# Performance work log

Measured on AMD Instinct MI355X. Metric: run time of the kernel, lower is better.

Reference implementation:

```python
import jax, jax.numpy as jnp
import numpy as np

B, N, M = 4, 2048, 2048
QUERY_DIM = 512
CONTEXT_DIM = 512
HEADS = 8
DIM_HEAD = 64
INNER = HEADS * DIM_HEAD  # 512
SCALE = DIM_HEAD ** -0.5


def setup_inputs() -> dict:
    key = jax.random.key(0)
    ks = jax.random.split(key, 7)
    x = jax.random.normal(ks[0], (B, N, QUERY_DIM), dtype=jnp.float32)
    context = jax.random.normal(ks[1], (B, M, CONTEXT_DIM), dtype=jnp.float32)
    mask = jax.random.randint(ks[2], (B, M), 0, 2) > 0  # bool key mask
    # Kaiming-uniform-ish init scale, like nn.Linear defaults
    Wq = jax.random.uniform(ks[3], (QUERY_DIM, INNER), dtype=jnp.float32,
                            minval=-1, maxval=1) * (QUERY_DIM ** -0.5)
    Wkv = jax.random.uniform(ks[4], (CONTEXT_DIM, 2 * INNER), dtype=jnp.float32,
                             minval=-1, maxval=1) * (CONTEXT_DIM ** -0.5)
    Wo = jax.random.uniform(ks[5], (INNER, QUERY_DIM), dtype=jnp.float32,
                            minval=-1, maxval=1) * (INNER ** -0.5)
    bo = jax.random.uniform(ks[6], (QUERY_DIM,), dtype=jnp.float32,
                            minval=-1, maxval=1) * (INNER ** -0.5)
    return {"x": x, "context": context, "mask": mask,
            "Wq": Wq, "Wkv": Wkv, "Wo": Wo, "bo": bo}


def reference(x, context, mask, Wq, Wkv, Wo, bo):
    # projections (no bias for q/kv, bias for out — as in the torch module)
    q = x @ Wq                       # [b, n, inner]
    kv = context @ Wkv               # [b, m, 2*inner]
    k, v = jnp.split(kv, 2, axis=-1)
    # split heads: b n (h d) -> b h n d
    def split_heads(t):
        b, n, _ = t.shape
        return t.reshape(b, n, HEADS, DIM_HEAD).transpose(0, 2, 1, 3)
    q, k, v = split_heads(q), split_heads(k), split_heads(v)
    sim = jnp.einsum('bhid,bhjd->bhij', q, k) * SCALE  # [b, h, n, m]
    max_neg = -jnp.finfo(sim.dtype).max
    sim = jnp.where(mask[:, None, None, :], sim, max_neg)
    attn = jax.nn.softmax(sim, axis=-1)
    out = jnp.einsum('bhij,bhjd->bhid', attn, v)       # [b, h, n, d]
    out = out.transpose(0, 2, 1, 3).reshape(x.shape[0], x.shape[1], INNER)
    return out @ Wo + bo
```

## Files before the change

### kernel.cpp

```cpp
#include <hip/hip_runtime.h>
#include <hip/hip_bf16.h>
#include <cstddef>

typedef __attribute__((ext_vector_type(8))) short short8;
typedef __attribute__((ext_vector_type(4))) float f32x4;

__device__ inline unsigned short f2bf(float f) {
  unsigned int u = __float_as_uint(f);
  u += 0x7fffu + ((u >> 16) & 1u);
  return (unsigned short)(u >> 16);
}
__device__ inline unsigned int pkbf(float a, float b) {
  __hip_bfloat162 h = __float22bfloat162_rn(make_float2(a, b));
  union { __hip_bfloat162 h2; unsigned int u; } cv;
  cv.h2 = h;
  return cv.u;
}

__global__ __launch_bounds__(256) void prep_kernel(
    const float* __restrict__ Wq, const float* __restrict__ Wkv,
    const float* __restrict__ Wo, const int* __restrict__ mask,
    unsigned short* __restrict__ Wq_t, unsigned short* __restrict__ Wkv_t,
    unsigned short* __restrict__ Wo_t, unsigned int* __restrict__ pmask) {
  const int z = blockIdx.z;
  if (z == 3) {
    if (blockIdx.y != 0) return;
    int idx = blockIdx.x * 256 + threadIdx.x;
    int bb = idx >> 10, rem = idx & 1023;
    int g = rem >> 5, rem2 = rem & 31;
    int lqv = rem2 >> 3, e = rem2 & 7;
    int ct = e >> 1, half = e & 1;
    int key0 = g * 64 + half * 32 + lqv * 8 + 2 * ct;
    const int* mb = mask + bb * 2048;
    pmask[idx] = (mb[key0] ? 0xFFFFu : 0u) | (mb[key0 + 1] ? 0xFFFF0000u : 0u);
    return;
  }
  const float* src = (z == 0) ? Wq : (z == 1) ? Wkv : Wo;
  unsigned short* dst = (z == 0) ? Wq_t : (z == 1) ? Wkv_t : Wo_t;
  const int R = 512, C = (z == 1) ? 1024 : 512;
  if (blockIdx.x * 64 >= C) return;
  __shared__ float tile[64][65];
  int c0 = blockIdx.x * 64, r0 = blockIdx.y * 64;
  int tx = threadIdx.x & 63, ty = threadIdx.x >> 6;
  for (int i = ty; i < 64; i += 4)
    tile[i][tx] = src[(size_t)(r0 + i) * C + c0 + tx];
  __syncthreads();
  for (int i = ty; i < 64; i += 4)
    dst[(size_t)(c0 + i) * R + r0 + tx] = f2bf(tile[tx][i]);
}

__global__ __launch_bounds__(256) void proj_kernel(
    const float* __restrict__ x, const float* __restrict__ context,
    const unsigned short* __restrict__ Wq_t, const unsigned short* __restrict__ Wkv_t,
    unsigned short* __restrict__ qb, unsigned short* __restrict__ kb,
    unsigned short* __restrict__ vtb, float qscale) {
  __shared__ unsigned short As[128][72];
  __shared__ unsigned short Bs[128][72];
  const int bid = blockIdx.x;
  const bool isq = bid < 256;
  const int lid = isq ? bid : bid - 256;
  const float* Af = isq ? x : context;
  const unsigned short* Bt = isq ? Wq_t : Wkv_t;
  const int bn = (isq ? (lid & 3) : (lid & 7)) * 128;
  const int bm = (isq ? (lid >> 2) : (lid >> 3)) * 128;
  const int K = 512;
  const int tid = threadIdx.x;
  const int wave = tid >> 6, lane = tid & 63;
  const int wr = (wave >> 1) * 64, wc = (wave & 1) * 64;
  const int l15 = lane & 15, lq = lane >> 4;
  const int sr = tid >> 3, sc = (tid & 7) * 8;
  f32x4 acc[4][4] = {};

  for (int k0 = 0; k0 < K; k0 += 64) {
    __syncthreads();
#pragma unroll
    for (int p = 0; p < 4; ++p) {
      int r = sr + p * 32;
      const float4 f0 = *(const float4*)(Af + (size_t)(bm + r) * K + k0 + sc);
      const float4 f1 = *(const float4*)(Af + (size_t)(bm + r) * K + k0 + sc + 4);
      uint4 u;
      u.x = pkbf(f0.x, f0.y);
      u.y = pkbf(f0.z, f0.w);
      u.z = pkbf(f1.x, f1.y);
      u.w = pkbf(f1.z, f1.w);
      *(uint4*)(&As[r][sc]) = u;
      *(uint4*)(&Bs[r][sc]) = *(const uint4*)(Bt + (size_t)(bn + r) * K + k0 + sc);
    }
    __syncthreads();
#pragma unroll
    for (int kk = 0; kk < 2; ++kk) {
      short8 af[4], bfr[4];
#pragma unroll
      for (int mt = 0; mt < 4; ++mt)
        af[mt] = *(const short8*)(&As[wr + mt * 16 + l15][kk * 32 + lq * 8]);
#pragma unroll
      for (int nt = 0; nt < 4; ++nt)
        bfr[nt] = *(const short8*)(&Bs[wc + nt * 16 + l15][kk * 32 + lq * 8]);
#pragma unroll
      for (int mt = 0; mt < 4; ++mt)
#pragma unroll
        for (int nt = 0; nt < 4; ++nt)
          acc[mt][nt] = __builtin_amdgcn_mfma_f32_16x16x32_bf16(af[mt], bfr[nt], acc[mt][nt], 0, 0, 0);
    }
  }

#pragma unroll
  for (int mt = 0; mt < 4; ++mt)
#pragma unroll
    for (int nt = 0; nt < 4; ++nt) {
      int row0 = bm + wr + mt * 16 + lq * 4;
      int col = bn + wc + nt * 16 + l15;
      if (isq) {
#pragma unroll
        for (int j = 0; j < 4; ++j)
          qb[(size_t)(row0 + j) * 512 + col] = f2bf(acc[mt][nt][j] * qscale);
      } else if (col < 512) {
#pragma unroll
        for (int j = 0; j < 4; ++j)
          kb[(size_t)(row0 + j) * 512 + col] = f2bf(acc[mt][nt][j]);
      } else {
        int bb = row0 >> 11, m = row0 & 2047;
        int hd = col - 512;
        uint2 w;
        w.x = pkbf(acc[mt][nt][0], acc[mt][nt][1]);
        w.y = pkbf(acc[mt][nt][2], acc[mt][nt][3]);
        *(uint2*)(vtb + ((size_t)bb * 512 + hd) * 2048 + m) = w;
      }
    }
}

__global__ __launch_bounds__(256) void outproj_kernel(
    const unsigned short* __restrict__ Ab, const unsigned short* __restrict__ Bt,
    float* __restrict__ C0, const float* __restrict__ bias) {
  __shared__ unsigned short As[64][72];
  __shared__ unsigned short Bs[128][72];
  const int bm = blockIdx.y * 64, bn = blockIdx.x * 128;
  const int K = 512, N = 512;
  const int tid = threadIdx.x;
  const int wave = tid >> 6, lane = tid & 63;
  const int wr = (wave >> 1) * 32, wc = (wave & 1) * 64;
  const int l15 = lane & 15, lq = lane >> 4;
  const int sr = tid >> 3, sc = (tid & 7) * 8;
  f32x4 acc[2][4] = {};

  for (int k0 = 0; k0 < K; k0 += 64) {
    __syncthreads();
#pragma unroll
    for (int p = 0; p < 2; ++p)
      *(uint4*)(&As[sr + p * 32][sc]) = *(const uint4*)(Ab + (size_t)(bm + sr + p * 32) * K + k0 + sc);
#pragma unroll
    for (int p = 0; p < 4; ++p)
      *(uint4*)(&Bs[sr + p * 32][sc]) = *(const uint4*)(Bt + (size_t)(bn + sr + p * 32) * K + k0 + sc);
    __syncthreads();
#pragma unroll
    for (int kk = 0; kk < 2; ++kk) {
      short8 af[2], bfr[4];
#pragma unroll
      for (int mt = 0; mt < 2; ++mt)
        af[mt] = *(const short8*)(&As[wr + mt * 16 + l15][kk * 32 + lq * 8]);
#pragma unroll
      for (int nt = 0; nt < 4; ++nt)
        bfr[nt] = *(const short8*)(&Bs[wc + nt * 16 + l15][kk * 32 + lq * 8]);
#pragma unroll
      for (int mt = 0; mt < 2; ++mt)
#pragma unroll
        for (int nt = 0; nt < 4; ++nt)
          acc[mt][nt] = __builtin_amdgcn_mfma_f32_16x16x32_bf16(af[mt], bfr[nt], acc[mt][nt], 0, 0, 0);
    }
  }

#pragma unroll
  for (int mt = 0; mt < 2; ++mt)
#pragma unroll
    for (int nt = 0; nt < 4; ++nt) {
      int row0 = bm + wr + mt * 16 + lq * 4;
      int col = bn + wc + nt * 16 + l15;
#pragma unroll
      for (int j = 0; j < 4; ++j)
        C0[(size_t)(row0 + j) * N + col] = acc[mt][nt][j] + bias[col];
    }
}

__global__ __launch_bounds__(256, 3) void attn_kernel(
    const unsigned short* __restrict__ Q, const unsigned short* __restrict__ Kb,
    const unsigned short* __restrict__ Vt, const unsigned int* __restrict__ pmask,
    unsigned short* __restrict__ O) {
  __shared__ unsigned short Ks[2][64][72];
  __shared__ unsigned short Vs[2][64][72];
  const int b = blockIdx.x >> 3, h = blockIdx.x & 7;
  const int tid = threadIdx.x, lane = tid & 63;
  const int wave = tid >> 6;
  const int l15 = lane & 15, lq = lane >> 4;
  const int wrow = blockIdx.y * 128 + wave * 32;

  const unsigned short* Qr0 = Q + (size_t)(b * 2048 + wrow + l15) * 512 + h * 64;
  const unsigned short* Qr1 = Q + (size_t)(b * 2048 + wrow + 16 + l15) * 512 + h * 64;
  short8 q00 = *(const short8*)(Qr0 + lq * 8);
  short8 q01 = *(const short8*)(Qr0 + 32 + lq * 8);
  short8 q10 = *(const short8*)(Qr1 + lq * 8);
  short8 q11 = *(const short8*)(Qr1 + 32 + lq * 8);

  const short8 vones = {0x3F80, 0x3F80, 0x3F80, 0x3F80,
                        0x3F80, 0x3F80, 0x3F80, 0x3F80};

  f32x4 o0[4] = {}, o1[4] = {};
  f32x4 ol0 = {}, ol1 = {};

  const unsigned short* Kg = Kb + (size_t)b * 2048 * 512 + h * 64;
  const unsigned short* Vg = Vt + (size_t)(b * 8 + h) * 64 * 2048;
  const unsigned int* Pm = pmask + b * 1024;

  const int str = tid >> 3;
  const int stc = (tid & 7) * 8;
  const int kprow = ((str & 7) >> 1) * 16 + ((str >> 3) & 3) * 4 + (str & 1);

  uint4 krA0 = *(const uint4*)(Kg + (size_t)str * 512 + stc);
  uint4 krA1 = *(const uint4*)(Kg + (size_t)(str + 32) * 512 + stc);
  uint4 krB0 = *(const uint4*)(Kg + (size_t)(64 + str) * 512 + stc);
  uint4 krB1 = *(const uint4*)(Kg + (size_t)(64 + str + 32) * 512 + stc);
  uint4 vrA0 = *(const uint4*)(Vg + (size_t)str * 2048 + stc);
  uint4 vrA1 = *(const uint4*)(Vg + (size_t)(str + 32) * 2048 + stc);
  uint4 vrB0 = *(const uint4*)(Vg + (size_t)str * 2048 + 64 + stc);
  uint4 vrB1 = *(const uint4*)(Vg + (size_t)(str + 32) * 2048 + 64 + stc);

  for (int mb = 0; mb < 2048; mb += 128) {
    __syncthreads();
    *(uint4*)(&Ks[0][kprow][stc])     = krA0;
    *(uint4*)(&Ks[0][kprow + 2][stc]) = krA1;
    *(uint4*)(&Ks[1][kprow][stc])     = krB0;
    *(uint4*)(&Ks[1][kprow + 2][stc]) = krB1;
    *(uint4*)(&Vs[0][str][stc])       = vrA0;
    *(uint4*)(&Vs[0][str + 32][stc])  = vrA1;
    *(uint4*)(&Vs[1][str][stc])       = vrB0;
    *(uint4*)(&Vs[1][str + 32][stc])  = vrB1;
    __syncthreads();
    if (mb + 128 < 2048) {
      const int nx = mb + 128;
      krA0 = *(const uint4*)(Kg + (size_t)(nx + str) * 512 + stc);
      krA1 = *(const uint4*)(Kg + (size_t)(nx + str + 32) * 512 + stc);
      krB0 = *(const uint4*)(Kg + (size_t)(nx + 64 + str) * 512 + stc);
      krB1 = *(const uint4*)(Kg + (size_t)(nx + 64 + str + 32) * 512 + stc);
      vrA0 = *(const uint4*)(Vg + (size_t)str * 2048 + nx + stc);
      vrA1 = *(const uint4*)(Vg + (size_t)(str + 32) * 2048 + nx + stc);
      vrB0 = *(const uint4*)(Vg + (size_t)str * 2048 + nx + 64 + stc);
      vrB1 = *(const uint4*)(Vg + (size_t)(str + 32) * 2048 + nx + 64 + stc);
    }

#pragma unroll
    for (int g = 0; g < 2; ++g) {
      const uint4 m0 = *(const uint4*)(Pm + ((mb >> 6) + g) * 32 + lq * 8);
      const uint4 m1 = *(const uint4*)(Pm + ((mb >> 6) + g) * 32 + lq * 8 + 4);

      f32x4 s0[4] = {}, s1[4] = {};
      __builtin_amdgcn_s_setprio(1);
#pragma unroll
      for (int ct = 0; ct < 4; ++ct) {
        short8 kf = *(const short8*)(&Ks[g][ct * 16 + l15][lq * 8]);
        s0[ct] = __builtin_amdgcn_mfma_f32_16x16x32_bf16(kf, q00, s0[ct], 0, 0, 0);
        s1[ct] = __builtin_amdgcn_mfma_f32_16x16x32_bf16(kf, q10, s1[ct], 0, 0, 0);
      }
#pragma unroll
      for (int ct = 0; ct < 4; ++ct) {
        short8 kf = *(const short8*)(&Ks[g][ct * 16 + l15][32 + lq * 8]);
        s0[ct] = __builtin_amdgcn_mfma_f32_16x16x32_bf16(kf, q01, s0[ct], 0, 0, 0);
        s1[ct] = __builtin_amdgcn_mfma_f32_16x16x32_bf16(kf, q11, s1[ct], 0, 0, 0);
      }
      __builtin_amdgcn_s_setprio(0);

      unsigned int xp0[4][2], xp1[4][2];
#pragma unroll
      for (int ct = 0; ct < 4; ++ct) {
        float a0 = __builtin_amdgcn_exp2f(s0[ct][0]);
        float a1 = __builtin_amdgcn_exp2f(s0[ct][1]);
        float a2 = __builtin_amdgcn_exp2f(s0[ct][2]);
        float a3 = __builtin_amdgcn_exp2f(s0[ct][3]);
        xp0[ct][0] = pkbf(a0, a1);
        xp0[ct][1] = pkbf(a2, a3);
        float c0 = __builtin_amdgcn_exp2f(s1[ct][0]);
        float c1 = __builtin_amdgcn_exp2f(s1[ct][1]);
        float c2 = __builtin_amdgcn_exp2f(s1[ct][2]);
        float c3 = __builtin_amdgcn_exp2f(s1[ct][3]);
        xp1[ct][0] = pkbf(c0, c1);
        xp1[ct][1] = pkbf(c2, c3);
      }

      xp0[0][0] &= m0.x; xp0[0][1] &= m0.y; xp0[1][0] &= m0.z; xp0[1][1] &= m0.w;
      xp0[2][0] &= m1.x; xp0[2][1] &= m1.y; xp0[3][0] &= m1.z; xp0[3][1] &= m1.w;
      xp1[0][0] &= m0.x; xp1[0][1] &= m0.y; xp1[1][0] &= m0.z; xp1[1][1] &= m0.w;
      xp1[2][0] &= m1.x; xp1[2][1] &= m1.y; xp1[3][0] &= m1.z; xp1[3][1] &= m1.w;

      __builtin_amdgcn_s_setprio(1);
#pragma unroll
      for (int kk = 0; kk < 2; ++kk) {
        union { unsigned int u[4]; short8 s8; } pc0, pc1;
        pc0.u[0] = xp0[0][kk]; pc0.u[1] = xp0[1][kk];
        pc0.u[2] = xp0[2][kk]; pc0.u[3] = xp0[3][kk];
        pc1.u[0] = xp1[0][kk]; pc1.u[1] = xp1[1][kk];
        pc1.u[2] = xp1[2][kk]; pc1.u[3] = xp1[3][kk];
#pragma unroll
        for (int dt = 0; dt < 4; ++dt) {
          short8 vf = *(const short8*)(&Vs[g][dt * 16 + l15][kk * 32 + lq * 8]);
          o0[dt] = __builtin_amdgcn_mfma_f32_16x16x32_bf16(vf, pc0.s8, o0[dt], 0, 0, 0);
          o1[dt] = __builtin_amdgcn_mfma_f32_16x16x32_bf16(vf, pc1.s8, o1[dt], 0, 0, 0);
        }
        ol0 = __builtin_amdgcn_mfma_f32_16x16x32_bf16(vones, pc0.s8, ol0, 0, 0, 0);
        ol1 = __builtin_amdgcn_mfma_f32_16x16x32_bf16(vones, pc1.s8, ol1, 0, 0, 0);
      }
      __builtin_amdgcn_s_setprio(0);
    }
  }

  float rl0 = 1.0f / ol0[0], rl1 = 1.0f / ol1[0];
  unsigned short* Or0 = O + (size_t)(b * 2048 + wrow + l15) * 512 + h * 64;
  unsigned short* Or1 = O + (size_t)(b * 2048 + wrow + 16 + l15) * 512 + h * 64;
#pragma unroll
  for (int dt = 0; dt < 4; ++dt) {
    *(unsigned int*)(Or0 + dt * 16 + lq * 4)     = pkbf(o0[dt][0] * rl0, o0[dt][1] * rl0);
    *(unsigned int*)(Or0 + dt * 16 + lq * 4 + 2) = pkbf(o0[dt][2] * rl0, o0[dt][3] * rl0);
    *(unsigned int*)(Or1 + dt * 16 + lq * 4)     = pkbf(o1[dt][0] * rl1, o1[dt][1] * rl1);
    *(unsigned int*)(Or1 + dt * 16 + lq * 4 + 2) = pkbf(o1[dt][2] * rl1, o1[dt][3] * rl1);
  }
}

extern "C" void kernel_launch(void* const* d_in, const int* in_sizes, int n_in,
                              void* d_out, int out_size, void* d_ws, size_t ws_size,
                              hipStream_t stream) {
  const float* x       = (const float*)d_in[0];
  const float* context = (const float*)d_in[1];
  const int*   mask    = (const int*)d_in[2];
  const float* Wq      = (const float*)d_in[3];
  const float* Wkv     = (const float*)d_in[4];
  const float* Wo      = (const float*)d_in[5];
  const float* bo      = (const float*)d_in[6];
  float* out = (float*)d_out;

  char* ws = (char*)d_ws;
  unsigned short* Wq_t  = (unsigned short*)(ws + 0);
  unsigned short* Wkv_t = (unsigned short*)(ws + 524288);
  unsigned short* Wo_t  = (unsigned short*)(ws + 1572864);
  unsigned short* qb    = (unsigned short*)(ws + 2097152);
  unsigned short* kb    = (unsigned short*)(ws + 10485760);
  unsigned short* vtb   = (unsigned short*)(ws + 18874368);
  unsigned short* ab    = (unsigned short*)(ws + 27262976);
  unsigned int* pmask   = (unsigned int*)(ws + 35651584);

  const float QSCALE = 0.125f * 1.44269504088896f;

  prep_kernel<<<dim3(16, 8, 4), 256, 0, stream>>>(Wq, Wkv, Wo, mask,
                                                  Wq_t, Wkv_t, Wo_t, pmask);
  proj_kernel<<<dim3(768), 256, 0, stream>>>(x, context, Wq_t, Wkv_t,
                                             qb, kb, vtb, QSCALE);
  attn_kernel<<<dim3(32, 16), 256, 0, stream>>>(qb, kb, vtb, pmask, ab);
  outproj_kernel<<<dim3(4, 128), 256, 0, stream>>>(ab, Wo_t, out, bo);
}
```

Before: 106.5 us.

## Split attention over key halves and merge partials in output projection

The attention kernel is split along the key dimension into two halves (grid z=2), each writing unnormalized bf16 partial outputs and row sums. The output projection then merges the two partials and normalizes while loading its A tile. Launch bounds rise to 4 blocks per CU and the setprio hints are removed. This doubles the number of attention blocks to fill more CUs, at the cost of extra partial-output traffic and merge arithmetic in outproj. It relies on softmax having no max subtraction, so partial sums can simply be added.

```diff
diff --git a/kernel.cpp b/kernel.cpp
--- a/kernel.cpp
+++ b/kernel.cpp
@@ -15,6 +15,12 @@
   union { __hip_bfloat162 h2; unsigned int u; } cv;
   cv.h2 = h;
   return cv.u;
+}
+__device__ inline float bf2f_lo(unsigned int u) {
+  return __uint_as_float(u << 16);
+}
+__device__ inline float bf2f_hi(unsigned int u) {
+  return __uint_as_float(u & 0xFFFF0000u);
 }
 
 __global__ __launch_bounds__(256) void prep_kernel(
@@ -130,7 +136,8 @@
 }
 
 __global__ __launch_bounds__(256) void outproj_kernel(
-    const unsigned short* __restrict__ Ab, const unsigned short* __restrict__ Bt,
+    const unsigned short* __restrict__ poA, const unsigned short* __restrict__ poB,
+    const float* __restrict__ ls, const unsigned short* __restrict__ Bt,
     float* __restrict__ C0, const float* __restrict__ bias) {
   __shared__ unsigned short As[64][72];
   __shared__ unsigned short Bs[128][72];
@@ -144,10 +151,22 @@
   f32x4 acc[2][4] = {};
 
   for (int k0 = 0; k0 < K; k0 += 64) {
-    __syncthreads();
-#pragma unroll
-    for (int p = 0; p < 2; ++p)
-      *(uint4*)(&As[sr + p * 32][sc]) = *(const uint4*)(Ab + (size_t)(bm + sr + p * 32) * K + k0 + sc);
+    const int h = k0 >> 6;
+    __syncthreads();
+#pragma unroll
+    for (int p = 0; p < 2; ++p) {
+      int row = bm + sr + p * 32;
+      uint4 ua = *(const uint4*)(poA + (size_t)row * 512 + k0 + sc);
+      uint4 ub = *(const uint4*)(poB + (size_t)row * 512 + k0 + sc);
+      float l = ls[(size_t)h * 8192 + row] + ls[65536 + (size_t)h * 8192 + row];
+      float rl = 1.0f / l;
+      uint4 u;
+      u.x = pkbf((bf2f_lo(ua.x) + bf2f_lo(ub.x)) * rl, (bf2f_hi(ua.x) + bf2f_hi(ub.x)) * rl);
+      u.y = pkbf((bf2f_lo(ua.y) + bf2f_lo(ub.y)) * rl, (bf2f_hi(ua.y) + bf2f_hi(ub.y)) * rl);
+      u.z = pkbf((bf2f_lo(ua.z) + bf2f_lo(ub.z)) * rl, (bf2f_hi(ua.z) + bf2f_hi(ub.z)) * rl);
+      u.w = pkbf((bf2f_lo(ua.w) + bf2f_lo(ub.w)) * rl, (bf2f_hi(ua.w) + bf2f_hi(ub.w)) * rl);
+      *(uint4*)(&As[sr + p * 32][sc]) = u;
+    }
 #pragma unroll
     for (int p = 0; p < 4; ++p)
       *(uint4*)(&Bs[sr + p * 32][sc]) = *(const uint4*)(Bt + (size_t)(bn + sr + p * 32) * K + k0 + sc);
@@ -181,13 +200,15 @@
     }
 }
 
-__global__ __launch_bounds__(256, 3) void attn_kernel(
+__global__ __launch_bounds__(256, 4) void attn_kernel(
     const unsigned short* __restrict__ Q, const unsigned short* __restrict__ Kb,
     const unsigned short* __restrict__ Vt, const unsigned int* __restrict__ pmask,
-    unsigned short* __restrict__ O) {
+    unsigned short* __restrict__ poA, unsigned short* __restrict__ poB,
+    float* __restrict__ ls) {
   __shared__ unsigned short Ks[2][64][72];
   __shared__ unsigned short Vs[2][64][72];
   const int b = blockIdx.x >> 3, h = blockIdx.x & 7;
+  const int z = blockIdx.z;
   const int tid = threadIdx.x, lane = tid & 63;
   const int wave = tid >> 6;
   const int l15 = lane & 15, lq = lane >> 4;
@@ -214,16 +235,18 @@
   const int stc = (tid & 7) * 8;
   const int kprow = ((str & 7) >> 1) * 16 + ((str >> 3) & 3) * 4 + (str & 1);
 
-  uint4 krA0 = *(const uint4*)(Kg + (size_t)str * 512 + stc);
-  uint4 krA1 = *(const uint4*)(Kg + (size_t)(str + 32) * 512 + stc);
-  uint4 krB0 = *(const uint4*)(Kg + (size_t)(64 + str) * 512 + stc);
-  uint4 krB1 = *(const uint4*)(Kg + (size_t)(64 + str + 32) * 512 + stc);
-  uint4 vrA0 = *(const uint4*)(Vg + (size_t)str * 2048 + stc);
-  uint4 vrA1 = *(const uint4*)(Vg + (size_t)(str + 32) * 2048 + stc);
-  uint4 vrB0 = *(const uint4*)(Vg + (size_t)str * 2048 + 64 + stc);
-  uint4 vrB1 = *(const uint4*)(Vg + (size_t)(str + 32) * 2048 + 64 + stc);
-
-  for (int mb = 0; mb < 2048; mb += 128) {
+  const int mb0 = z << 10;
+
+  uint4 krA0 = *(const uint4*)(Kg + (size_t)(mb0 + str) * 512 + stc);
+  uint4 krA1 = *(const uint4*)(Kg + (size_t)(mb0 + str + 32) * 512 + stc);
+  uint4 krB0 = *(const uint4*)(Kg + (size_t)(mb0 + 64 + str) * 512 + stc);
+  uint4 krB1 = *(const uint4*)(Kg + (size_t)(mb0 + 64 + str + 32) * 512 + stc);
+  uint4 vrA0 = *(const uint4*)(Vg + (size_t)str * 2048 + mb0 + stc);
+  uint4 vrA1 = *(const uint4*)(Vg + (size_t)(str + 32) * 2048 + mb0 + stc);
+  uint4 vrB0 = *(const uint4*)(Vg + (size_t)str * 2048 + mb0 + 64 + stc);
+  uint4 vrB1 = *(const uint4*)(Vg + (size_t)(str + 32) * 2048 + mb0 + 64 + stc);
+
+  for (int mb = mb0; mb < mb0 + 1024; mb += 128) {
     __syncthreads();
     *(uint4*)(&Ks[0][kprow][stc])     = krA0;
     *(uint4*)(&Ks[0][kprow + 2][stc]) = krA1;
@@ -234,7 +257,7 @@
     *(uint4*)(&Vs[1][str][stc])       = vrB0;
     *(uint4*)(&Vs[1][str + 32][stc])  = vrB1;
     __syncthreads();
-    if (mb + 128 < 2048) {
+    if (mb + 128 < mb0 + 1024) {
       const int nx = mb + 128;
       krA0 = *(const uint4*)(Kg + (size_t)(nx + str) * 512 + stc);
       krA1 = *(const uint4*)(Kg + (size_t)(nx + str + 32) * 512 + stc);
@@ -252,7 +275,6 @@
       const uint4 m1 = *(const uint4*)(Pm + ((mb >> 6) + g) * 32 + lq * 8 + 4);
 
       f32x4 s0[4] = {}, s1[4] = {};
-      __builtin_amdgcn_s_setprio(1);
 #pragma unroll
       for (int ct = 0; ct < 4; ++ct) {
         short8 kf = *(const short8*)(&Ks[g][ct * 16 + l15][lq * 8]);
@@ -265,7 +287,6 @@
         s0[ct] = __builtin_amdgcn_mfma_f32_16x16x32_bf16(kf, q01, s0[ct], 0, 0, 0);
         s1[ct] = __builtin_amdgcn_mfma_f32_16x16x32_bf16(kf, q11, s1[ct], 0, 0, 0);
       }
-      __builtin_amdgcn_s_setprio(0);
 
       unsigned int xp0[4][2], xp1[4][2];
 #pragma unroll
@@ -289,7 +310,6 @@
       xp1[0][0] &= m0.x; xp1[0][1] &= m0.y; xp1[1][0] &= m0.z; xp1[1][1] &= m0.w;
       xp1[2][0] &= m1.x; xp1[2][1] &= m1.y; xp1[3][0] &= m1.z; xp1[3][1] &= m1.w;
 
-      __builtin_amdgcn_s_setprio(1);
 #pragma unroll
       for (int kk = 0; kk < 2; ++kk) {
         union { unsigned int u[4]; short8 s8; } pc0, pc1;
@@ -306,19 +326,22 @@
         ol0 = __builtin_amdgcn_mfma_f32_16x16x32_bf16(vones, pc0.s8, ol0, 0, 0, 0);
         ol1 = __builtin_amdgcn_mfma_f32_16x16x32_bf16(vones, pc1.s8, ol1, 0, 0, 0);
       }
-      __builtin_amdgcn_s_setprio(0);
-    }
-  }
-
-  float rl0 = 1.0f / ol0[0], rl1 = 1.0f / ol1[0];
-  unsigned short* Or0 = O + (size_t)(b * 2048 + wrow + l15) * 512 + h * 64;
-  unsigned short* Or1 = O + (size_t)(b * 2048 + wrow + 16 + l15) * 512 + h * 64;
+    }
+  }
+
+  unsigned short* po = z ? poB : poA;
+  unsigned short* Or0 = po + (size_t)(b * 2048 + wrow + l15) * 512 + h * 64;
+  unsigned short* Or1 = po + (size_t)(b * 2048 + wrow + 16 + l15) * 512 + h * 64;
 #pragma unroll
   for (int dt = 0; dt < 4; ++dt) {
-    *(unsigned int*)(Or0 + dt * 16 + lq * 4)     = pkbf(o0[dt][0] * rl0, o0[dt][1] * rl0);
-    *(unsigned int*)(Or0 + dt * 16 + lq * 4 + 2) = pkbf(o0[dt][2] * rl0, o0[dt][3] * rl0);
-    *(unsigned int*)(Or1 + dt * 16 + lq * 4)     = pkbf(o1[dt][0] * rl1, o1[dt][1] * rl1);
-    *(unsigned int*)(Or1 + dt * 16 + lq * 4 + 2) = pkbf(o1[dt][2] * rl1, o1[dt][3] * rl1);
+    *(unsigned int*)(Or0 + dt * 16 + lq * 4)     = pkbf(o0[dt][0], o0[dt][1]);
+    *(unsigned int*)(Or0 + dt * 16 + lq * 4 + 2) = pkbf(o0[dt][2], o0[dt][3]);
+    *(unsigned int*)(Or1 + dt * 16 + lq * 4)     = pkbf(o1[dt][0], o1[dt][1]);
+    *(unsigned int*)(Or1 + dt * 16 + lq * 4 + 2) = pkbf(o1[dt][2], o1[dt][3]);
+  }
+  if (lq == 0) {
+    ls[((size_t)z * 8 + h) * 8192 + b * 2048 + wrow + l15]      = ol0[0];
+    ls[((size_t)z * 8 + h) * 8192 + b * 2048 + wrow + 16 + l15] = ol1[0];
   }
 }
 
@@ -341,8 +364,10 @@
   unsigned short* qb    = (unsigned short*)(ws + 2097152);
   unsigned short* kb    = (unsigned short*)(ws + 10485760);
   unsigned short* vtb   = (unsigned short*)(ws + 18874368);
-  unsigned short* ab    = (unsigned short*)(ws + 27262976);
-  unsigned int* pmask   = (unsigned int*)(ws + 35651584);
+  unsigned short* poA   = (unsigned short*)(ws + 27262976);
+  unsigned short* poB   = (unsigned short*)(ws + 35651584);
+  unsigned int* pmask   = (unsigned int*)(ws + 44040192);
+  float* ls             = (float*)(ws + 44056576);
 
   const float QSCALE = 0.125f * 1.44269504088896f;
 
@@ -350,6 +375,7 @@
                                                   Wq_t, Wkv_t, Wo_t, pmask);
   proj_kernel<<<dim3(768), 256, 0, stream>>>(x, context, Wq_t, Wkv_t,
                                              qb, kb, vtb, QSCALE);
-  attn_kernel<<<dim3(32, 16), 256, 0, stream>>>(qb, kb, vtb, pmask, ab);
-  outproj_kernel<<<dim3(4, 128), 256, 0, stream>>>(ab, Wo_t, out, bo);
-}
+  attn_kernel<<<dim3(32, 16, 2), 256, 0, stream>>>(qb, kb, vtb, pmask,
+                                                   poA, poB, ls);
+  outproj_kernel<<<dim3(4, 128), 256, 0, stream>>>(poA, poB, ls, Wo_t, out, bo);
+}
```

Result: slower. 140.0 us (+31.4%).
